# Optimization experiments

Hardware: AMD Instinct MI355X
Metric: run time of the kernel (lower is better)

Reference implementation:

```python
import jax, jax.numpy as jnp
import numpy as np
from jax import lax

AR_VOCAB = 25
EN_VOCAB = 25
N_CLASSES = 1 + AR_VOCAB + EN_VOCAB + AR_VOCAB * EN_VOCAB  # full_table id layout
NEG = -jnp.inf
BIG_NEG = -1e30  # acts as log(0) in float32 (exp underflows to exactly 0) but keeps grads finite
T_LEN = 256
V_LEN = 256


def setup_inputs() -> dict:
    key = jax.random.key(0)
    k1, k2 = jax.random.split(key)
    ar_sent = jax.random.randint(k1, (1, T_LEN), 0, AR_VOCAB)
    en_sent = jax.random.randint(k2, (1, V_LEN), 0, EN_VOCAB)
    # self.weights = log(uniform) over target classes
    weights = jnp.full((N_CLASSES,), -jnp.log(jnp.float32(N_CLASSES)), dtype=jnp.float32)
    return {"ar_sent": ar_sent, "en_sent": en_sent, "weights": weights}


def _chain(c, m):
    """Solve a[0]=c[0]; a[i]=logaddexp(c[i], m[i]+a[i-1]) in parallel.
    a[i] = s[i] + logcumsumexp(c - s)[i] with s = prefix sums of m (s[0]=0)."""
    s = jnp.concatenate([jnp.zeros((1,), c.dtype), jnp.cumsum(m[1:])])
    return s + lax.associative_scan(jnp.logaddexp, c - s)


def _safe_lse(x, axis):
    """Stable logsumexp that returns -inf (with zero gradient) on empty/-inf slices."""
    m = lax.stop_gradient(jnp.max(x, axis=axis, keepdims=True))
    m = jnp.where(jnp.isfinite(m), m, 0.0)
    s = jnp.sum(jnp.exp(x - m), axis=axis)
    ok = s > 0
    return jnp.squeeze(m, axis=axis) + jnp.where(ok, jnp.log(jnp.where(ok, s, 1.0)), NEG)


def _forward(ar, en, weights):
    # ar: [T] int, en: [V] int, weights: [C] log-probs
    T, V = ar.shape[0], en.shape[0]
    del_ids = 1 + ar                                               # [T]
    ins_ids = 1 + AR_VOCAB + en                                    # [V]
    sub_ids = 1 + AR_VOCAB + EN_VOCAB + EN_VOCAB * ar[:, None] + en[None, :]  # [T,V]
    w_del = weights[del_ids]   # [T]
    w_ins = weights[ins_ids]   # [V]
    w_sub = weights[sub_ids]   # [T,V]

    # ---- alpha DP (forward lattice) ----
    # row 0: alpha[0,0]=0, alpha[0,v]=alpha[0,v-1]+w_ins[v]
    c0 = jnp.full((V,), BIG_NEG, weights.dtype).at[0].set(0.0)
    row0 = _chain(c0, w_ins)

    def fstep(prev, xs):
        wd, ws = xs  # w_del[t] scalar, w_sub[t,:] [V]
        # c[v] = logaddexp(w_del[t]+alpha[t-1,v], w_sub[t,v]+alpha[t-1,v-1]); v=0 has no sub term
        c = jnp.concatenate([(wd + prev[0])[None],
                             jnp.logaddexp(wd + prev[1:], ws[1:] + prev[:-1])])
        row = _chain(c, w_ins)  # adds within-row insertion recurrence
        return row, row

    _, frows = lax.scan(fstep, row0, (w_del[1:], w_sub[1:]))
    alpha = jnp.concatenate([row0[None], frows], axis=0)  # [T,V]

    # ---- beta DP (backward lattice) ----
    m_rev = w_ins[::-1]
    cT = jnp.full((V,), BIG_NEG, weights.dtype).at[-1].set(0.0)
    rowT = _chain(cT[::-1], m_rev)[::-1]

    def bstep(nxt, xs):
        wd, ws = xs
        # c[v] = logaddexp(w_del[t]+beta[t+1,v], w_sub[t,v]+beta[t+1,v+1]); v=V-1 has no sub term
        c = jnp.concatenate([jnp.logaddexp(wd + nxt[:-1], ws[:-1] + nxt[1:]),
                             (wd + nxt[-1])[None]])
        row = _chain(c[::-1], m_rev)[::-1]  # beta[t,v] += w_ins[v]+beta[t,v+1] recurrence
        return row, row

    _, brows = lax.scan(bstep, rowT, (w_del[:-1], w_sub[:-1]), reverse=True)
    beta = jnp.concatenate([brows, rowT[None]], axis=0)  # [T,V]

    # ---- expected edit-operation counts (log space) ----
    cls = jnp.arange(N_CLASSES)
    w = weights[None, None, :]
    md = jnp.where(del_ids[1:, None, None] == cls, 0.0, NEG)   # [T-1,1,C] one-hot log mask
    mi = jnp.where(ins_ids[None, 1:, None] == cls, 0.0, NEG)   # [1,V-1,C]
    ms = jnp.where(sub_ids[1:, 1:, None] == cls, 0.0, NEG)     # [T-1,V-1,C]
    ed = alpha[:-1, :, None] + w + md + beta[1:, :, None]      # expected deletions
    ei = alpha[:, :-1, None] + w + mi + beta[:, 1:, None]      # expected insertions
    es = alpha[:-1, :-1, None] + w + ms + beta[1:, 1:, None]   # expected substitutions
    return _safe_lse(jnp.stack([_safe_lse(ed, (0, 1)),
                                _safe_lse(ei, (0, 1)),
                                _safe_lse(es, (0, 1))]), 0)    # [C]


def reference(ar_sent, en_sent, weights):
    return _forward(ar_sent[0], en_sent[0], weights)
```

## Files before the change

kernel.cpp:

```cpp
#include <hip/hip_runtime.h>
#include <math.h>

#define NCLS 676
#define NEG_SENTINEL -3.0e38f
#define LN2F 0.6931471805599453f
#define JPAD 768
#define ROWS 768
#define QIP_OFF 692
#define WSE_OFF 1460
#define SHM_FLOATS (WSE_OFF + 25 * JPAD)
#define MAGIC 0x13579BDFu

struct f4u { float x, y, z, w; };

__device__ __forceinline__ float dpp_shr1(float x) {
  return __int_as_float(
      __builtin_amdgcn_update_dpp(0, __float_as_int(x), 0x138, 0xF, 0xF, false));
}
__device__ __forceinline__ float dpp_shl1(float x) {
  return __int_as_float(
      __builtin_amdgcn_update_dpp(0, __float_as_int(x), 0x130, 0xF, 0xF, false));
}
__device__ __forceinline__ int dpp_shr1_i(int x) {
  return __builtin_amdgcn_update_dpp(0, x, 0x138, 0xF, 0xF, false);
}
__device__ __forceinline__ int dpp_shl1_i(int x) {
  return __builtin_amdgcn_update_dpp(0, x, 0x130, 0xF, 0xF, false);
}
__device__ __forceinline__ float pow2c(int d) {
  d = min(max(d, -126), 126);
  return __int_as_float((d + 127) << 23);
}

__global__ __launch_bounds__(256) void k_fused(const int* __restrict__ ar,
                                               const int* __restrict__ en,
                                               const float* __restrict__ wts,
                                               float* __restrict__ aD,
                                               float* __restrict__ bD,
                                               int* __restrict__ aEb,
                                               int* __restrict__ bEb,
                                               float* __restrict__ S,
                                               unsigned* __restrict__ flags,
                                               int* __restrict__ wcnt,
                                               float* __restrict__ out) {
  const int tid = threadIdx.x;
  __shared__ alignas(16) float shm[SHM_FLOATS];

  if (blockIdx.x >= 2) {
    float* bins = shm;
    int* ctl = (int*)(shm + 680);
    __shared__ int lastf;
    for (int c = tid; c < NCLS; c += 256) bins[c] = 0.f;
    if (tid == 0) ctl[0] = 0;
    __syncthreads();
    if (tid == 0) {
      while (__hip_atomic_load(&flags[0], __ATOMIC_RELAXED,
                               __HIP_MEMORY_SCOPE_AGENT) != MAGIC ||
             __hip_atomic_load(&flags[1], __ATOMIC_RELAXED,
                               __HIP_MEMORY_SCOPE_AGENT) != MAGIC)
        __builtin_amdgcn_s_sleep(16);
      (void)__hip_atomic_load(&flags[0], __ATOMIC_ACQUIRE,
                              __HIP_MEMORY_SCOPE_AGENT);
      __hip_atomic_store(&ctl[0], 1, __ATOMIC_RELEASE,
                         __HIP_MEMORY_SCOPE_WORKGROUP);
    } else if (tid >= 64) {
      float x = 1.0f + (float)tid;
      while (__hip_atomic_load(&ctl[0], __ATOMIC_RELAXED,
                               __HIP_MEMORY_SCOPE_WORKGROUP) == 0) {
#pragma unroll
        for (int z = 0; z < 128; ++z) x = fmaf(x, 1.0000001f, 1.0e-7f);
      }
      if (x == 123.456f) atomicAdd(&S[0], 0.f);
    }
    __syncthreads();
    const float M = __logf(aD[510 * ROWS + 256 + 255]) +
                    (float)aEb[63 * 64 + 63] * LN2F + 16.0f;
    const int j = tid;
    const int e = en[j];
#pragma unroll
    for (int u = 0; u < 4; ++u) {
      const int d = ((int)blockIdx.x - 2) * 4 + u;
      if (d <= 510) {
        const int i = d - j;
        if (i >= 0 && i <= 255) {
          const float bM = bD[d * ROWS + 256 + j];
          if (bM > 0.f) {
            const int bEx =
                (d == 510) ? 0 : bEb[((509 - d) >> 3) * 64 + (i >> 2)];
            const float lb = __logf(bM) + (float)bEx * LN2F - M;
            const int a = ar[i];
            if (i >= 1) {
              float aM = aD[(d - 1) * ROWS + 256 + j];
              if (aM > 0.f) {
                int eA =
                    (d == 1) ? 0 : aEb[((d - 2) >> 3) * 64 + ((i - 1) >> 2)];
                float L = __logf(aM) + (float)eA * LN2F + lb;
                atomicAdd(&bins[1 + a], __expf(fminf(L, 0.f)));
              }
            }
            if (j >= 1) {
              float aM = aD[(d - 1) * ROWS + 256 + j - 1];
              if (aM > 0.f) {
                int eA = (d == 1) ? 0 : aEb[((d - 2) >> 3) * 64 + (i >> 2)];
                float L = __logf(aM) + (float)eA * LN2F + lb;
                atomicAdd(&bins[26 + e], __expf(fminf(L, 0.f)));
              }
              if (i >= 1) {
                float aM2 = aD[(d - 2) * ROWS + 256 + j - 1];
                if (aM2 > 0.f) {
                  int eA2 =
                      (d == 2) ? 0 : aEb[((d - 3) >> 3) * 64 + ((i - 1) >> 2)];
                  float L2 = __logf(aM2) + (float)eA2 * LN2F + lb;
                  atomicAdd(&bins[51 + 25 * a + e], __expf(fminf(L2, 0.f)));
                }
              }
            }
          }
        }
      }
    }
    __syncthreads();
    for (int c = tid; c < NCLS; c += 256)
      if (bins[c] != 0.f) atomicAdd(&S[c], bins[c]);
    if (tid == 0) {
      __threadfence();
      lastf = (atomicAdd(wcnt, 1) == 127) ? 1 : 0;
    }
    __syncthreads();
    if (lastf == 0) return;
    __threadfence();
    for (int c = tid; c < NCLS; c += 256) {
      float s = __hip_atomic_load(&S[c], __ATOMIC_ACQUIRE,
                                  __HIP_MEMORY_SCOPE_AGENT);
      out[c] =
          (c != 0 && s > 0.f) ? (wts[c] + M + __logf(s)) : NEG_SENTINEL;
    }
    return;
  }

  float* pw = shm;
  float* qip = shm + QIP_OFF;
  float* wsE = shm + WSE_OFF;
  for (int c = tid; c < NCLS; c += 256) pw[c] = __expf(wts[c]);
  {
    float4* z = (float4*)(shm + NCLS);
    const int nz = (SHM_FLOATS - NCLS) / 4;
    for (int t = tid; t < nz; t += 256) z[t] = make_float4(0.f, 0.f, 0.f, 0.f);
  }
  if (blockIdx.x == 0) {
    for (int c = tid; c < NCLS; c += 256) S[c] = 0.f;
    if (tid == 0) *wcnt = 0;
  }
  __syncthreads();
  {
    int j = tid;
    int ee = en[j];
    qip[255 + j] = pw[26 + ee];
#pragma unroll
    for (int a = 0; a < 25; ++a) wsE[a * JPAD + 255 + j] = pw[51 + 25 * a + ee];
  }
  __syncthreads();
  if (tid >= 64) return;
  const int lane = tid;

  const int i0 = 4 * lane;
  float wdl[4];
  const float* rowp[4];
#pragma unroll
  for (int k = 0; k < 4; ++k) {
    int a = ar[i0 + k];
    wdl[k] = pw[1 + a];
    rowp[k] = wsE + a * JPAD;
  }
  float P1[4] = {0.f, 0.f, 0.f, 0.f};
  float P2[4] = {0.f, 0.f, 0.f, 0.f};
  int e1 = 0;

  if (blockIdx.x == 0) {
    if (lane == 0) { P1[0] = 1.f; aD[0 * ROWS + 256] = 1.f; }
    int e0 = 252 - i0;
    float* sp = aD + ROWS + 256 + (1 - i0 - 3);
    int* ep = aEb + lane;
    float W0[4][12], Q0[12], W1[4][12], Q1[12];

#define LOAD_A(EB, W, Q)                                                   \
  {                                                                        \
    _Pragma("unroll") for (int k = 0; k < 4; ++k) {                        \
      const float4* p = (const float4*)(rowp[k] + (EB));                   \
      float4 va = p[0], vb = p[1], vc = p[2];                              \
      W[k][0] = va.x; W[k][1] = va.y; W[k][2] = va.z; W[k][3] = va.w;      \
      W[k][4] = vb.x; W[k][5] = vb.y; W[k][6] = vb.z; W[k][7] = vb.w;      \
      W[k][8] = vc.x; W[k][9] = vc.y; W[k][10] = vc.z; W[k][11] = vc.w;    \
    }                                                                      \
    const float4* q = (const float4*)(qip + (EB));                         \
    float4 qa = q[0], qb = q[1], qc = q[2];                                \
    Q[0] = qa.x; Q[1] = qa.y; Q[2] = qa.z; Q[3] = qa.w;                    \
    Q[4] = qb.x; Q[5] = qb.y; Q[6] = qb.z; Q[7] = qb.w;                    \
    Q[8] = qc.x; Q[9] = qc.y; Q[10] = qc.z; Q[11] = qc.w;                  \
  }

#define PROC_A(W, Q)                                                       \
  {                                                                        \
    *ep = e1; ep += 64;                                                    \
    int t1e = dpp_shr1_i(e1);                                              \
    float f1n = pow2c(t1e - e1);                                           \
    _Pragma("unroll") for (int u = 0; u < 8; ++u) {                        \
      float pm1 = dpp_shr1(P1[3]) * f1n;                                   \
      float pm2 = dpp_shr1(P2[3]) * f1n;                                   \
      float cu[4];                                                         \
      _Pragma("unroll") for (int k = 0; k < 4; ++k) {                      \
        float a1 = (k == 0) ? pm1 : P1[k - 1];                             \
        float a2 = (k == 0) ? pm2 : P2[k - 1];                             \
        cu[k] = fmaf(wdl[k], a1,                                           \
                     fmaf(W[k][4 + u - k], a2, Q[4 + u - k] * P1[k]));     \
      }                                                                    \
      *(f4u*)sp = f4u{cu[3], cu[2], cu[1], cu[0]};                         \
      sp += ROWS + 1;                                                      \
      _Pragma("unroll") for (int k = 0; k < 4; ++k) {                      \
        P2[k] = P1[k]; P1[k] = cu[k];                                      \
      }                                                                    \
    }                                                                      \
    float m = fmaxf(fmaxf(P1[0], P1[1]), fmaxf(P1[2], P1[3]));             \
    int ex = (m > 0.f) ? ((__float_as_int(m) >> 23) - 126) : (t1e - e1);   \
    float sc = pow2c(-ex);                                                 \
    _Pragma("unroll") for (int k = 0; k < 4; ++k) {                        \
      P1[k] *= sc; P2[k] *= sc;                                            \
    }                                                                      \
    e1 += ex;                                                              \
  }

    LOAD_A(e0, W0, Q0);
    for (int it = 0; it < 31; ++it) {
      LOAD_A(e0 + 8, W1, Q1);
      PROC_A(W0, Q0);
      LOAD_A(e0 + 16, W0, Q0);
      PROC_A(W1, Q1);
      e0 += 16;
    }
    LOAD_A(e0 + 8, W1, Q1);
    PROC_A(W0, Q0);
    PROC_A(W1, Q1);
  } else {
    if (lane == 63) P1[3] = 1.f;
    if (lane == 0) bD[510 * ROWS + 256 + 255] = 1.f;
    int e0 = 752 - i0;
    float* sp = bD + 509 * ROWS + 256 + (509 - i0 - 3);
    int* ep = bEb + lane;
    float W0[4][16], Q0[16], W1[4][16], Q1[16];

#define LOAD_B(EB, W, Q)                                                   \
  {                                                                        \
    _Pragma("unroll") for (int k = 0; k < 4; ++k) {                        \
      const float4* p = (const float4*)(rowp[k] + (EB));                   \
      float4 va = p[0], vb = p[1], vc = p[2], vd = p[3];                   \
      W[k][0] = va.x; W[k][1] = va.y; W[k][2] = va.z; W[k][3] = va.w;      \
      W[k][4] = vb.x; W[k][5] = vb.y; W[k][6] = vb.z; W[k][7] = vb.w;      \
      W[k][8] = vc.x; W[k][9] = vc.y; W[k][10] = vc.z; W[k][11] = vc.w;    \
      W[k][12] = vd.x; W[k][13] = vd.y; W[k][14] = vd.z; W[k][15] = vd.w;  \
    }                                                                      \
    const float4* q = (const float4*)(qip + (EB));                         \
    float4 qa = q[0], qb = q[1], qc = q[2], qd = q[3];                     \
    Q[0] = qa.x; Q[1] = qa.y; Q[2] = qa.z; Q[3] = qa.w;                    \
    Q[4] = qb.x; Q[5] = qb.y; Q[6] = qb.z; Q[7] = qb.w;                    \
    Q[8] = qc.x; Q[9] = qc.y; Q[10] = qc.z; Q[11] = qc.w;                  \
    Q[12] = qd.x; Q[13] = qd.y; Q[14] = qd.z; Q[15] = qd.w;                \
  }

#define PROC_B(W, Q)                                                       \
  {                                                                        \
    *ep = e1; ep += 64;                                                    \
    int t1e = dpp_shl1_i(e1);                                              \
    float f1n = pow2c(t1e - e1);                                           \
    _Pragma("unroll") for (int u = 0; u < 8; ++u) {                        \
      float pm1 = dpp_shl1(P1[0]) * f1n;                                   \
      float pm2 = dpp_shl1(P2[0]) * f1n;                                   \
      float cu[4];                                                         \
      _Pragma("unroll") for (int k = 0; k < 4; ++k) {                      \
        float a1 = (k == 3) ? pm1 : P1[k + 1];                             \
        float a2 = (k == 3) ? pm2 : P2[k + 1];                             \
        cu[k] = fmaf(wdl[k], a1,                                           \
                     fmaf(W[k][12 - u - k], a2, Q[13 - u - k] * P1[k]));   \
      }                                                                    \
      *(f4u*)sp = f4u{cu[3], cu[2], cu[1], cu[0]};                         \
      sp -= ROWS + 1;                                                      \
      _Pragma("unroll") for (int k = 0; k < 4; ++k) {                      \
        P2[k] = P1[k]; P1[k] = cu[k];                                      \
      }                                                                    \
    }                                                                      \
    float m = fmaxf(fmaxf(P1[0], P1[1]), fmaxf(P1[2], P1[3]));             \
    int ex = (m > 0.f) ? ((__float_as_int(m) >> 23) - 126) : (t1e - e1);   \
    float sc = pow2c(-ex);                                                 \
    _Pragma("unroll") for (int k = 0; k < 4; ++k) {                        \
      P1[k] *= sc; P2[k] *= sc;                                            \
    }                                                                      \
    e1 += ex;                                                              \
  }

    LOAD_B(e0, W0, Q0);
    for (int it = 0; it < 31; ++it) {
      LOAD_B(e0 - 8, W1, Q1);
      PROC_B(W0, Q0);
      LOAD_B(e0 - 16, W0, Q0);
      PROC_B(W1, Q1);
      e0 -= 16;
    }
    LOAD_B(e0 - 8, W1, Q1);
    PROC_B(W0, Q0);
    PROC_B(W1, Q1);
  }

  __threadfence();
  if (lane == 0)
    __hip_atomic_store(&flags[blockIdx.x], MAGIC, __ATOMIC_RELEASE,
                       __HIP_MEMORY_SCOPE_AGENT);
}

extern "C" void kernel_launch(void* const* d_in, const int* in_sizes, int n_in,
                              void* d_out, int out_size, void* d_ws, size_t ws_size,
                              hipStream_t stream) {
  const int* ar = (const int*)d_in[0];
  const int* en = (const int*)d_in[1];
  const float* wts = (const float*)d_in[2];
  float* aD = (float*)d_ws;
  float* bDraw = aD + 514 * ROWS;
  float* bD = bDraw + 2 * ROWS;
  int* aEb = (int*)(bDraw + 514 * ROWS);
  int* bEb = aEb + 4096;
  float* S = (float*)(bEb + 4096);
  unsigned* flags = (unsigned*)(S + NCLS);
  int* wcnt = (int*)(flags + 2);
  k_fused<<<130, 256, 0, stream>>>(ar, en, wts, aD, bD, aEb, bEb, S, flags,
                                   wcnt, (float*)d_out);
}
```

Measured before the change: 98.85 us.

## Index DP buffers by anti-diagonal offset for aligned float4 stores; drop spin warmup

After: 98.53 us. Within noise of the previous version (-0.3%).

```diff
diff --git a/kernel.cpp b/kernel.cpp
--- a/kernel.cpp
+++ b/kernel.cpp
@@ -6,12 +6,11 @@
 #define LN2F 0.6931471805599453f
 #define JPAD 768
 #define ROWS 768
+#define CSH 259
 #define QIP_OFF 692
 #define WSE_OFF 1460
 #define SHM_FLOATS (WSE_OFF + 25 * JPAD)
 #define MAGIC 0x13579BDFu
-
-struct f4u { float x, y, z, w; };
 
 __device__ __forceinline__ float dpp_shr1(float x) {
   return __int_as_float(
@@ -48,11 +47,8 @@
 
   if (blockIdx.x >= 2) {
     float* bins = shm;
-    int* ctl = (int*)(shm + 680);
     __shared__ int lastf;
     for (int c = tid; c < NCLS; c += 256) bins[c] = 0.f;
-    if (tid == 0) ctl[0] = 0;
-    __syncthreads();
     if (tid == 0) {
       while (__hip_atomic_load(&flags[0], __ATOMIC_RELAXED,
                                __HIP_MEMORY_SCOPE_AGENT) != MAGIC ||
@@ -61,19 +57,9 @@
         __builtin_amdgcn_s_sleep(16);
       (void)__hip_atomic_load(&flags[0], __ATOMIC_ACQUIRE,
                               __HIP_MEMORY_SCOPE_AGENT);
-      __hip_atomic_store(&ctl[0], 1, __ATOMIC_RELEASE,
-                         __HIP_MEMORY_SCOPE_WORKGROUP);
-    } else if (tid >= 64) {
-      float x = 1.0f + (float)tid;
-      while (__hip_atomic_load(&ctl[0], __ATOMIC_RELAXED,
-                               __HIP_MEMORY_SCOPE_WORKGROUP) == 0) {
-#pragma unroll
-        for (int z = 0; z < 128; ++z) x = fmaf(x, 1.0000001f, 1.0e-7f);
-      }
-      if (x == 123.456f) atomicAdd(&S[0], 0.f);
     }
     __syncthreads();
-    const float M = __logf(aD[510 * ROWS + 256 + 255]) +
+    const float M = __logf(aD[510 * ROWS + 4]) +
                     (float)aEb[63 * 64 + 63] * LN2F + 16.0f;
     const int j = tid;
     const int e = en[j];
@@ -83,14 +69,14 @@
       if (d <= 510) {
         const int i = d - j;
         if (i >= 0 && i <= 255) {
-          const float bM = bD[d * ROWS + 256 + j];
+          const float bM = bD[d * ROWS + CSH - i];
           if (bM > 0.f) {
             const int bEx =
                 (d == 510) ? 0 : bEb[((509 - d) >> 3) * 64 + (i >> 2)];
             const float lb = __logf(bM) + (float)bEx * LN2F - M;
             const int a = ar[i];
             if (i >= 1) {
-              float aM = aD[(d - 1) * ROWS + 256 + j];
+              float aM = aD[(d - 1) * ROWS + CSH - (i - 1)];
               if (aM > 0.f) {
                 int eA =
                     (d == 1) ? 0 : aEb[((d - 2) >> 3) * 64 + ((i - 1) >> 2)];
@@ -99,14 +85,14 @@
               }
             }
             if (j >= 1) {
-              float aM = aD[(d - 1) * ROWS + 256 + j - 1];
+              float aM = aD[(d - 1) * ROWS + CSH - i];
               if (aM > 0.f) {
                 int eA = (d == 1) ? 0 : aEb[((d - 2) >> 3) * 64 + (i >> 2)];
                 float L = __logf(aM) + (float)eA * LN2F + lb;
                 atomicAdd(&bins[26 + e], __expf(fminf(L, 0.f)));
               }
               if (i >= 1) {
-                float aM2 = aD[(d - 2) * ROWS + 256 + j - 1];
+                float aM2 = aD[(d - 2) * ROWS + CSH - (i - 1)];
                 if (aM2 > 0.f) {
                   int eA2 =
                       (d == 2) ? 0 : aEb[((d - 3) >> 3) * 64 + ((i - 1) >> 2)];
@@ -177,9 +163,9 @@
   int e1 = 0;
 
   if (blockIdx.x == 0) {
-    if (lane == 0) { P1[0] = 1.f; aD[0 * ROWS + 256] = 1.f; }
+    if (lane == 0) { P1[0] = 1.f; aD[CSH] = 1.f; }
     int e0 = 252 - i0;
-    float* sp = aD + ROWS + 256 + (1 - i0 - 3);
+    float* sp = aD + ROWS + (CSH - i0 - 3);
     int* ep = aEb + lane;
     float W0[4][12], Q0[12], W1[4][12], Q1[12];
 
@@ -214,8 +200,8 @@
         cu[k] = fmaf(wdl[k], a1,                                           \
                      fmaf(W[k][4 + u - k], a2, Q[4 + u - k] * P1[k]));     \
       }                                                                    \
-      *(f4u*)sp = f4u{cu[3], cu[2], cu[1], cu[0]};                         \
-      sp += ROWS + 1;                                                      \
+      *(float4*)sp = make_float4(cu[3], cu[2], cu[1], cu[0]);              \
+      sp += ROWS;                                                          \
       _Pragma("unroll") for (int k = 0; k < 4; ++k) {                      \
         P2[k] = P1[k]; P1[k] = cu[k];                                      \
       }                                                                    \
@@ -242,9 +228,9 @@
     PROC_A(W1, Q1);
   } else {
     if (lane == 63) P1[3] = 1.f;
-    if (lane == 0) bD[510 * ROWS + 256 + 255] = 1.f;
+    if (lane == 0) bD[510 * ROWS + CSH - 255] = 1.f;
     int e0 = 752 - i0;
-    float* sp = bD + 509 * ROWS + 256 + (509 - i0 - 3);
+    float* sp = bD + 509 * ROWS + (CSH - i0 - 3);
     int* ep = bEb + lane;
     float W0[4][16], Q0[16], W1[4][16], Q1[16];
 
@@ -281,8 +267,8 @@
         cu[k] = fmaf(wdl[k], a1,                                           \
                      fmaf(W[k][12 - u - k], a2, Q[13 - u - k] * P1[k]));   \
       }                                                                    \
-      *(f4u*)sp = f4u{cu[3], cu[2], cu[1], cu[0]};                         \
-      sp -= ROWS + 1;                                                      \
+      *(float4*)sp = make_float4(cu[3], cu[2], cu[1], cu[0]);              \
+      sp -= ROWS;                                                          \
       _Pragma("unroll") for (int k = 0; k < 4; ++k) {                      \
         P2[k] = P1[k]; P1[k] = cu[k];                                      \
       }                                                                    \
```
